# Optimization experiments

Measured on AMD Instinct MI355X. Metric: run time of the kernel, lower is better.

The kernel has to match this reference:

```python
import jax, jax.numpy as jnp
import numpy as np

B, N, D, H = 4096, 257, 16, 128  # batch, agents(incl ego), input_dim, hidden_dim


def setup_inputs() -> dict:
    key = jax.random.key(0)
    k1, k2, k3, k4, k5, k6 = jax.random.split(key, 6)
    x = jax.random.normal(k1, (B, N, D), dtype=jnp.float32)
    # columns 6,7,8 are one-hot type flags (vehicle / pedestrian / barrier)
    tidx = jax.random.randint(k2, (B, N), 0, 3)
    onehot = jax.nn.one_hot(tidx, 3, dtype=jnp.float32)
    x = x.at[:, :, 6:9].set(onehot)
    # Linear params (torch convention: y = x @ W.T + b)
    W_fc = jax.random.normal(k3, (H, D), dtype=jnp.float32) / np.sqrt(D)
    b_fc = jax.random.normal(k4, (H,), dtype=jnp.float32) * 0.01
    W_agg = jax.random.normal(k5, (H, H), dtype=jnp.float32) / np.sqrt(H)
    b_agg = jax.random.normal(k6, (H,), dtype=jnp.float32) * 0.01
    return {"agent_tensor": x, "W_fc": W_fc, "b_fc": b_fc,
            "W_agg": W_agg, "b_agg": b_agg}


def reference(agent_tensor, W_fc, b_fc, W_agg, b_agg):
    x = agent_tensor.astype(jnp.float32)
    ego_pos = x[:, 0, :2]            # [B, 2]
    agents = x[:, 1:, :]             # [B, N-1, D]
    # distance-based weights
    dists = jnp.linalg.norm(agents[:, :, :2] - ego_pos[:, None, :], axis=-1)  # [B, N-1]
    w = 1.0 / (dists + 1.0)
    # vehicle flag multiplies weight by 5 (pedestrian/barrier multipliers are 1.0 -> no-op)
    w = jnp.where(agents[:, :, 6] == 1, w * 5.0, w)
    w = w / (jnp.sum(w, axis=-1, keepdims=True) + 1e-10)
    # per-agent embedding + weighted aggregation
    emb = jax.nn.relu(jnp.einsum('bnd,hd->bnh', agents, W_fc) + b_fc)  # [B, N-1, H]
    agg = jnp.einsum('bn,bnh->bh', w, emb)                              # [B, H]
    return jnp.einsum('bh,gh->bg', jax.nn.relu(agg), W_agg) + b_agg    # [B, H]
```

## Files before the change

### kernel.cpp

```cpp
#include <hip/hip_runtime.h>


typedef _Float16 half_t;
typedef half_t f16x4 __attribute__((ext_vector_type(4)));
typedef float f32x4 __attribute__((ext_vector_type(4)));

__global__ __launch_bounds__(256, 4) void agg_kernel(
    const float* __restrict__ x,
    const float* __restrict__ Wfc,
    const float* __restrict__ bfc,
    half_t* __restrict__ agg_out)
{
    const int t    = threadIdx.x;
    const int lane = t & 63;
    const int wv   = t >> 6;
    const int b    = blockIdx.x * 4 + wv;
    const int lr   = lane & 15;
    const int lc   = lane >> 4;

    __shared__ float wls[4][256];

    const float* xb = x + (size_t)b * (257 * 16);

    float dxv[4], dyv[4], f6[4];
    #pragma unroll
    for (int i = 0; i < 4; ++i) {
        const float* ar = xb + (size_t)(1 + lane + 64 * i) * 16;
        const float2 p = *(const float2*)ar;
        dxv[i] = p.x; dyv[i] = p.y; f6[i] = ar[6];
    }
    const float2 ego = *(const float2*)xb;

    f16x4 afr[16];
    #pragma unroll
    for (int tm = 0; tm < 16; ++tm) {
        const float4 av = *(const float4*)(xb + (size_t)(1 + tm * 16 + lr) * 16 + lc * 4);
        afr[tm] = (f16x4){(half_t)av.x, (half_t)av.y, (half_t)av.z, (half_t)av.w};
    }

    f16x4 bf[8];
    float cbias[8];
    #pragma unroll
    for (int ct = 0; ct < 8; ++ct) {
        const int col = ct * 16 + lr;
        const float4 v = *(const float4*)(Wfc + col * 16 + lc * 4);
        bf[ct] = (f16x4){(half_t)v.x, (half_t)v.y, (half_t)v.z, (half_t)v.w};
        cbias[ct] = bfc[col];
    }

    float wq[4];
    float wsum = 0.f;
    #pragma unroll
    for (int i = 0; i < 4; ++i) {
        const float dx = dxv[i] - ego.x, dy = dyv[i] - ego.y;
        float w = 1.0f / (sqrtf(dx * dx + dy * dy) + 1.0f);
        if (f6[i] == 1.0f) w *= 5.0f;
        wq[i] = w; wsum += w;
    }
    #pragma unroll
    for (int off = 32; off > 0; off >>= 1) wsum += __shfl_xor(wsum, off);
    const float inv = 1.0f / (wsum + 1e-10f);
    #pragma unroll
    for (int i = 0; i < 4; ++i) wls[wv][lane + 64 * i] = wq[i] * inv;

    float pacc[8] = {0.f, 0.f, 0.f, 0.f, 0.f, 0.f, 0.f, 0.f};
    #pragma unroll
    for (int tm = 0; tm < 16; ++tm) {
        const float4 w4 = *(const float4*)(&wls[wv][tm * 16 + lc * 4]);
        #pragma unroll
        for (int ct = 0; ct < 8; ++ct) {
            const f32x4 c = (f32x4){cbias[ct], cbias[ct], cbias[ct], cbias[ct]};
            const f32x4 d = __builtin_amdgcn_mfma_f32_16x16x16f16(afr[tm], bf[ct], c, 0, 0, 0);
            pacc[ct] = fmaf(w4.x, fmaxf(d[0], 0.f), pacc[ct]);
            pacc[ct] = fmaf(w4.y, fmaxf(d[1], 0.f), pacc[ct]);
            pacc[ct] = fmaf(w4.z, fmaxf(d[2], 0.f), pacc[ct]);
            pacc[ct] = fmaf(w4.w, fmaxf(d[3], 0.f), pacc[ct]);
        }
    }

    #pragma unroll
    for (int ct = 0; ct < 8; ++ct) {
        float p = pacc[ct];
        p += __shfl_xor(p, 16);
        p += __shfl_xor(p, 32);
        pacc[ct] = p;
    }
    if (lane < 16) {
        #pragma unroll
        for (int ct = 0; ct < 8; ++ct)
            agg_out[(size_t)b * 128 + ct * 16 + lane] = (half_t)fmaxf(pacc[ct], 0.f);
    }
}

__global__ __launch_bounds__(256) void out_kernel(
    const half_t* __restrict__ agg,
    const float* __restrict__ Wagg,
    const float* __restrict__ bagg,
    float* __restrict__ out)
{
    const int blk  = blockIdx.x;
    const int t    = threadIdx.x;
    const int lane = t & 63;
    const int wv   = t >> 6;
    const int lr   = lane & 15;
    const int lc   = lane >> 4;
    const int row0 = blk * 16;

    f32x4 acc[2];
    #pragma unroll
    for (int ci = 0; ci < 2; ++ci) {
        const int col = (wv * 2 + ci) * 16 + lr;
        const float bb = bagg[col];
        acc[ci] = (f32x4){bb, bb, bb, bb};
    }
    #pragma unroll
    for (int kk = 0; kk < 8; ++kk) {
        const int k0 = kk * 16 + lc * 4;
        const f16x4 a = *(const f16x4*)(agg + (size_t)(row0 + lr) * 128 + k0);
        #pragma unroll
        for (int ci = 0; ci < 2; ++ci) {
            const int col = (wv * 2 + ci) * 16 + lr;
            const float4 v = *(const float4*)(Wagg + col * 128 + k0);
            const f16x4 bfr = (f16x4){(half_t)v.x, (half_t)v.y, (half_t)v.z, (half_t)v.w};
            acc[ci] = __builtin_amdgcn_mfma_f32_16x16x16f16(a, bfr, acc[ci], 0, 0, 0);
        }
    }
    #pragma unroll
    for (int ci = 0; ci < 2; ++ci) {
        const int col = (wv * 2 + ci) * 16 + lr;
        #pragma unroll
        for (int j = 0; j < 4; ++j)
            out[(size_t)(row0 + lc * 4 + j) * 128 + col] = acc[ci][j];
    }
}

extern "C" void kernel_launch(void* const* d_in, const int* in_sizes, int n_in,
                              void* d_out, int out_size, void* d_ws, size_t ws_size,
                              hipStream_t stream) {
    const float* x    = (const float*)d_in[0];
    const float* Wfc  = (const float*)d_in[1];
    const float* bfc  = (const float*)d_in[2];
    const float* Wagg = (const float*)d_in[3];
    const float* bagg = (const float*)d_in[4];
    float* out = (float*)d_out;
    half_t* agg_ws = (half_t*)d_ws;

    agg_kernel<<<dim3(1024), dim3(256), 0, stream>>>(x, Wfc, bfc, agg_ws);
    out_kernel<<<dim3(256), dim3(256), 0, stream>>>(agg_ws, Wagg, bagg, out);
}
```

Baseline: 36.88 us.

## Defer weight normalization and stream agent tiles through a rotating prefetch buffer

The kernel now writes unnormalized distance weights to shared memory and applies the normalization after the MFMA loop, so the wave reduction no longer sits before the main compute. Agent tiles are loaded into a four-deep rotating register buffer and prefetched four tiles ahead, replacing the up-front load of all sixteen tiles. Bias vectors are also prebuilt outside the loop. The aim is to cut register pressure and overlap global loads with MFMA work, at the cost of a slightly different floating-point summation order.

After: 36.06 us. 1.02x faster.

```diff
diff --git a/kernel.cpp b/kernel.cpp
--- a/kernel.cpp
+++ b/kernel.cpp
@@ -22,55 +22,53 @@
 
     const float* xb = x + (size_t)b * (257 * 16);
 
-    float dxv[4], dyv[4], f6[4];
-    #pragma unroll
-    for (int i = 0; i < 4; ++i) {
-        const float* ar = xb + (size_t)(1 + lane + 64 * i) * 16;
-        const float2 p = *(const float2*)ar;
-        dxv[i] = p.x; dyv[i] = p.y; f6[i] = ar[6];
-    }
-    const float2 ego = *(const float2*)xb;
-
-    f16x4 afr[16];
-    #pragma unroll
-    for (int tm = 0; tm < 16; ++tm) {
-        const float4 av = *(const float4*)(xb + (size_t)(1 + tm * 16 + lr) * 16 + lc * 4);
-        afr[tm] = (f16x4){(half_t)av.x, (half_t)av.y, (half_t)av.z, (half_t)av.w};
+    float wq[4];
+    {
+        float2 p[4]; float f6[4];
+        #pragma unroll
+        for (int i = 0; i < 4; ++i) {
+            const float* ar = xb + (size_t)(1 + lane + 64 * i) * 16;
+            p[i] = *(const float2*)ar;
+            f6[i] = ar[6];
+        }
+        const float2 ego = *(const float2*)xb;
+        #pragma unroll
+        for (int i = 0; i < 4; ++i) {
+            const float dx = p[i].x - ego.x, dy = p[i].y - ego.y;
+            float w = 1.0f / (sqrtf(dx * dx + dy * dy) + 1.0f);
+            if (f6[i] == 1.0f) w *= 5.0f;
+            wq[i] = w;
+            wls[wv][lane + 64 * i] = w;
+        }
     }
 
     f16x4 bf[8];
-    float cbias[8];
+    f32x4 cvec[8];
     #pragma unroll
     for (int ct = 0; ct < 8; ++ct) {
         const int col = ct * 16 + lr;
         const float4 v = *(const float4*)(Wfc + col * 16 + lc * 4);
         bf[ct] = (f16x4){(half_t)v.x, (half_t)v.y, (half_t)v.z, (half_t)v.w};
-        cbias[ct] = bfc[col];
+        const float bb = bfc[col];
+        cvec[ct] = (f32x4){bb, bb, bb, bb};
     }
 
-    float wq[4];
-    float wsum = 0.f;
+    float pacc[8] = {0.f, 0.f, 0.f, 0.f, 0.f, 0.f, 0.f, 0.f};
+    float4 abuf[4];
     #pragma unroll
-    for (int i = 0; i < 4; ++i) {
-        const float dx = dxv[i] - ego.x, dy = dyv[i] - ego.y;
-        float w = 1.0f / (sqrtf(dx * dx + dy * dy) + 1.0f);
-        if (f6[i] == 1.0f) w *= 5.0f;
-        wq[i] = w; wsum += w;
-    }
-    #pragma unroll
-    for (int off = 32; off > 0; off >>= 1) wsum += __shfl_xor(wsum, off);
-    const float inv = 1.0f / (wsum + 1e-10f);
-    #pragma unroll
-    for (int i = 0; i < 4; ++i) wls[wv][lane + 64 * i] = wq[i] * inv;
+    for (int i = 0; i < 4; ++i)
+        abuf[i] = *(const float4*)(xb + (size_t)(1 + i * 16 + lr) * 16 + lc * 4);
 
-    float pacc[8] = {0.f, 0.f, 0.f, 0.f, 0.f, 0.f, 0.f, 0.f};
     #pragma unroll
     for (int tm = 0; tm < 16; ++tm) {
+        const float4 av = abuf[tm & 3];
+        if (tm < 12)
+            abuf[tm & 3] = *(const float4*)(xb + (size_t)(1 + (tm + 4) * 16 + lr) * 16 + lc * 4);
+        const f16x4 a = (f16x4){(half_t)av.x, (half_t)av.y, (half_t)av.z, (half_t)av.w};
         const float4 w4 = *(const float4*)(&wls[wv][tm * 16 + lc * 4]);
         #pragma unroll
         for (int ct = 0; ct < 8; ++ct) {
-            const f32x4 c = (f32x4){cbias[ct], cbias[ct], cbias[ct], cbias[ct]};
-            const f32x4 d = __builtin_amdgcn_mfma_f32_16x16x16f16(afr[tm], bf[ct], c, 0, 0, 0);
+            const f32x4 d = __builtin_amdgcn_mfma_f32_16x16x16f16(a, bf[ct], cvec[ct], 0, 0, 0);
             pacc[ct] = fmaf(w4.x, fmaxf(d[0], 0.f), pacc[ct]);
             pacc[ct] = fmaf(w4.y, fmaxf(d[1], 0.f), pacc[ct]);
             pacc[ct] = fmaf(w4.z, fmaxf(d[2], 0.f), pacc[ct]);
@@ -78,12 +76,17 @@
         }
     }
 
+    float wsum = wq[0] + wq[1] + wq[2] + wq[3];
+    #pragma unroll
+    for (int off = 32; off > 0; off >>= 1) wsum += __shfl_xor(wsum, off);
+    const float inv = 1.0f / (wsum + 1e-10f);
+
     #pragma unroll
     for (int ct = 0; ct < 8; ++ct) {
         float p = pacc[ct];
         p += __shfl_xor(p, 16);
         p += __shfl_xor(p, 32);
-        pacc[ct] = p;
+        pacc[ct] = p * inv;
     }
     if (lane < 16) {
         #pragma unroll
```

## Split agents across two waves, use 32x32 MFMA, defer normalization and bias

Applied to the files above, without the earlier changes.

Each batch row is now handled by two waves, each covering half of the 256 agents. The embedding uses the 32x32x16 f16 MFMA with a zero accumulator and clamps at -bias instead of adding the bias first. Each wave writes unnormalized partial sums and its weight sum to fp32 workspace. The second kernel combines the two halves, applies the normalization and the weighted bias (sum of weights is 1), then runs a 16x16x32 MFMA. The aim is more parallelism and less per-wave register and VALU work, at the cost of twice as much fp32 workspace traffic between the kernels.

Measured after the change: 30.47 us. 17.4% less time.

```diff
diff --git a/kernel.cpp b/kernel.cpp
--- a/kernel.cpp
+++ b/kernel.cpp
@@ -2,136 +2,159 @@
 
 
 typedef _Float16 half_t;
-typedef half_t f16x4 __attribute__((ext_vector_type(4)));
+typedef half_t f16x8 __attribute__((ext_vector_type(8)));
 typedef float f32x4 __attribute__((ext_vector_type(4)));
+typedef float f32x16 __attribute__((ext_vector_type(16)));
 
-__global__ __launch_bounds__(256, 4) void agg_kernel(
+__global__ __launch_bounds__(256, 5) void agg_kernel(
     const float* __restrict__ x,
     const float* __restrict__ Wfc,
     const float* __restrict__ bfc,
-    half_t* __restrict__ agg_out)
+    float* __restrict__ p_ws,
+    float* __restrict__ s_ws)
 {
     const int t    = threadIdx.x;
     const int lane = t & 63;
     const int wv   = t >> 6;
-    const int b    = blockIdx.x * 4 + wv;
-    const int lr   = lane & 15;
-    const int lc   = lane >> 4;
+    const int W    = blockIdx.x * 4 + wv;
+    const int b    = W >> 1;
+    const int hf   = W & 1;
+    const int lm   = lane & 31;
+    const int hi   = lane >> 5;
 
-    __shared__ float wls[4][256];
+    __shared__ float wls[4][128];
 
     const float* xb = x + (size_t)b * (257 * 16);
+    const int row0 = 1 + hf * 128;
 
-    float dxv[4], dyv[4], f6[4];
+    float4 a0[4], a1[4];
     #pragma unroll
-    for (int i = 0; i < 4; ++i) {
-        const float* ar = xb + (size_t)(1 + lane + 64 * i) * 16;
-        const float2 p = *(const float2*)ar;
-        dxv[i] = p.x; dyv[i] = p.y; f6[i] = ar[6];
+    for (int tm = 0; tm < 4; ++tm) {
+        const float* rp = xb + (size_t)(row0 + tm * 32 + lm) * 16 + hi * 8;
+        a0[tm] = *(const float4*)rp;
+        a1[tm] = *(const float4*)(rp + 4);
     }
+
+    f16x8 bfr[4];
+    #pragma unroll
+    for (int ct = 0; ct < 4; ++ct) {
+        const float* wp = Wfc + (size_t)(ct * 32 + lm) * 16 + hi * 8;
+        const float4 w0 = *(const float4*)wp;
+        const float4 w1 = *(const float4*)(wp + 4);
+        bfr[ct] = (f16x8){(half_t)w0.x, (half_t)w0.y, (half_t)w0.z, (half_t)w0.w,
+                          (half_t)w1.x, (half_t)w1.y, (half_t)w1.z, (half_t)w1.w};
+    }
+
+    float nb[4];
+    #pragma unroll
+    for (int ct = 0; ct < 4; ++ct) nb[ct] = -bfc[ct * 32 + lm];
+
     const float2 ego = *(const float2*)xb;
 
-    f16x4 afr[16];
-    #pragma unroll
-    for (int tm = 0; tm < 16; ++tm) {
-        const float4 av = *(const float4*)(xb + (size_t)(1 + tm * 16 + lr) * 16 + lc * 4);
-        afr[tm] = (f16x4){(half_t)av.x, (half_t)av.y, (half_t)av.z, (half_t)av.w};
-    }
-
-    f16x4 bf[8];
-    float cbias[8];
-    #pragma unroll
-    for (int ct = 0; ct < 8; ++ct) {
-        const int col = ct * 16 + lr;
-        const float4 v = *(const float4*)(Wfc + col * 16 + lc * 4);
-        bf[ct] = (f16x4){(half_t)v.x, (half_t)v.y, (half_t)v.z, (half_t)v.w};
-        cbias[ct] = bfc[col];
-    }
-
-    float wq[4];
     float wsum = 0.f;
-    #pragma unroll
-    for (int i = 0; i < 4; ++i) {
-        const float dx = dxv[i] - ego.x, dy = dyv[i] - ego.y;
-        float w = 1.0f / (sqrtf(dx * dx + dy * dy) + 1.0f);
-        if (f6[i] == 1.0f) w *= 5.0f;
-        wq[i] = w; wsum += w;
+    if (hi == 0) {
+        #pragma unroll
+        for (int tm = 0; tm < 4; ++tm) {
+            const float dx = a0[tm].x - ego.x;
+            const float dy = a0[tm].y - ego.y;
+            float w = 1.0f / (sqrtf(dx * dx + dy * dy) + 1.0f);
+            if (a1[tm].z == 1.0f) w *= 5.0f;
+            wls[wv][tm * 32 + lm] = w;
+            wsum += w;
+        }
     }
     #pragma unroll
     for (int off = 32; off > 0; off >>= 1) wsum += __shfl_xor(wsum, off);
-    const float inv = 1.0f / (wsum + 1e-10f);
+
+    f16x8 afr[4];
     #pragma unroll
-    for (int i = 0; i < 4; ++i) wls[wv][lane + 64 * i] = wq[i] * inv;
+    for (int tm = 0; tm < 4; ++tm)
+        afr[tm] = (f16x8){(half_t)a0[tm].x, (half_t)a0[tm].y, (half_t)a0[tm].z, (half_t)a0[tm].w,
+                          (half_t)a1[tm].x, (half_t)a1[tm].y, (half_t)a1[tm].z, (half_t)a1[tm].w};
 
-    float pacc[8] = {0.f, 0.f, 0.f, 0.f, 0.f, 0.f, 0.f, 0.f};
+    float pacc[4] = {0.f, 0.f, 0.f, 0.f};
     #pragma unroll
-    for (int tm = 0; tm < 16; ++tm) {
-        const float4 w4 = *(const float4*)(&wls[wv][tm * 16 + lc * 4]);
+    for (int tm = 0; tm < 4; ++tm) {
+        float4 w4[4];
         #pragma unroll
-        for (int ct = 0; ct < 8; ++ct) {
-            const f32x4 c = (f32x4){cbias[ct], cbias[ct], cbias[ct], cbias[ct]};
-            const f32x4 d = __builtin_amdgcn_mfma_f32_16x16x16f16(afr[tm], bf[ct], c, 0, 0, 0);
-            pacc[ct] = fmaf(w4.x, fmaxf(d[0], 0.f), pacc[ct]);
-            pacc[ct] = fmaf(w4.y, fmaxf(d[1], 0.f), pacc[ct]);
-            pacc[ct] = fmaf(w4.z, fmaxf(d[2], 0.f), pacc[ct]);
-            pacc[ct] = fmaf(w4.w, fmaxf(d[3], 0.f), pacc[ct]);
+        for (int q = 0; q < 4; ++q)
+            w4[q] = *(const float4*)(&wls[wv][tm * 32 + q * 8 + hi * 4]);
+        #pragma unroll
+        for (int ct = 0; ct < 4; ++ct) {
+            f32x16 zc = {};
+            const f32x16 d = __builtin_amdgcn_mfma_f32_32x32x16_f16(afr[tm], bfr[ct], zc, 0, 0, 0);
+            #pragma unroll
+            for (int r = 0; r < 16; ++r)
+                pacc[ct] = fmaf(w4[r >> 2][r & 3], fmaxf(d[r], nb[ct]), pacc[ct]);
         }
     }
 
     #pragma unroll
-    for (int ct = 0; ct < 8; ++ct) {
-        float p = pacc[ct];
-        p += __shfl_xor(p, 16);
-        p += __shfl_xor(p, 32);
-        pacc[ct] = p;
-    }
-    if (lane < 16) {
+    for (int ct = 0; ct < 4; ++ct) pacc[ct] += __shfl_xor(pacc[ct], 32);
+    if (hi == 0) {
+        float* pp = p_ws + ((size_t)b * 2 + hf) * 128;
         #pragma unroll
-        for (int ct = 0; ct < 8; ++ct)
-            agg_out[(size_t)b * 128 + ct * 16 + lane] = (half_t)fmaxf(pacc[ct], 0.f);
+        for (int ct = 0; ct < 4; ++ct) pp[ct * 32 + lm] = pacc[ct];
+        if (lane == 0) s_ws[b * 2 + hf] = wsum;
     }
 }
 
-__global__ __launch_bounds__(256) void out_kernel(
-    const half_t* __restrict__ agg,
+__global__ __launch_bounds__(256, 4) void out_kernel(
+    const float* __restrict__ p_ws,
+    const float* __restrict__ s_ws,
+    const float* __restrict__ bfc,
     const float* __restrict__ Wagg,
     const float* __restrict__ bagg,
     float* __restrict__ out)
 {
-    const int blk  = blockIdx.x;
     const int t    = threadIdx.x;
     const int lane = t & 63;
     const int wv   = t >> 6;
+    const int j    = blockIdx.x * 4 + wv;
+    const int mt   = j >> 3;
+    const int ct   = j & 7;
     const int lr   = lane & 15;
-    const int lc   = lane >> 4;
-    const int row0 = blk * 16;
+    const int lq   = lane >> 4;
 
-    f32x4 acc[2];
+    const int brow = mt * 16 + lr;
+    const float2 s2 = *(const float2*)(s_ws + brow * 2);
+    const float inv = 1.0f / (s2.x + s2.y + 1e-10f);
+
+    const int col = ct * 16 + lr;
+    const float bb = bagg[col];
+    f32x4 acc = (f32x4){bb, bb, bb, bb};
+
+    const float* pbase = p_ws + (size_t)brow * 256;
+    const float* wrow  = Wagg + (size_t)col * 128;
+
     #pragma unroll
-    for (int ci = 0; ci < 2; ++ci) {
-        const int col = (wv * 2 + ci) * 16 + lr;
-        const float bb = bagg[col];
-        acc[ci] = (f32x4){bb, bb, bb, bb};
+    for (int kk = 0; kk < 4; ++kk) {
+        const int k0 = kk * 32 + lq * 8;
+        const float4 p00 = *(const float4*)(pbase + k0);
+        const float4 p01 = *(const float4*)(pbase + k0 + 4);
+        const float4 p10 = *(const float4*)(pbase + 128 + k0);
+        const float4 p11 = *(const float4*)(pbase + 128 + k0 + 4);
+        const float4 bf0 = *(const float4*)(bfc + k0);
+        const float4 bf1 = *(const float4*)(bfc + k0 + 4);
+        const f16x8 afr = (f16x8){
+            (half_t)fmaxf(fmaf(p00.x + p10.x, inv, bf0.x), 0.f),
+            (half_t)fmaxf(fmaf(p00.y + p10.y, inv, bf0.y), 0.f),
+            (half_t)fmaxf(fmaf(p00.z + p10.z, inv, bf0.z), 0.f),
+            (half_t)fmaxf(fmaf(p00.w + p10.w, inv, bf0.w), 0.f),
+            (half_t)fmaxf(fmaf(p01.x + p11.x, inv, bf1.x), 0.f),
+            (half_t)fmaxf(fmaf(p01.y + p11.y, inv, bf1.y), 0.f),
+            (half_t)fmaxf(fmaf(p01.z + p11.z, inv, bf1.z), 0.f),
+            (half_t)fmaxf(fmaf(p01.w + p11.w, inv, bf1.w), 0.f)};
+        const float4 wg0 = *(const float4*)(wrow + k0);
+        const float4 wg1 = *(const float4*)(wrow + k0 + 4);
+        const f16x8 bfr = (f16x8){(half_t)wg0.x, (half_t)wg0.y, (half_t)wg0.z, (half_t)wg0.w,
+                                  (half_t)wg1.x, (half_t)wg1.y, (half_t)wg1.z, (half_t)wg1.w};
+        acc = __builtin_amdgcn_mfma_f32_16x16x32_f16(afr, bfr, acc, 0, 0, 0);
     }
+
     #pragma unroll
-    for (int kk = 0; kk < 8; ++kk) {
-        const int k0 = kk * 16 + lc * 4;
-        const f16x4 a = *(const f16x4*)(agg + (size_t)(row0 + lr) * 128 + k0);
-        #pragma unroll
-        for (int ci = 0; ci < 2; ++ci) {
-            const int col = (wv * 2 + ci) * 16 + lr;
-            const float4 v = *(const float4*)(Wagg + col * 128 + k0);
-            const f16x4 bfr = (f16x4){(half_t)v.x, (half_t)v.y, (half_t)v.z, (half_t)v.w};
-            acc[ci] = __builtin_amdgcn_mfma_f32_16x16x16f16(a, bfr, acc[ci], 0, 0, 0);
-        }
-    }
-    #pragma unroll
-    for (int ci = 0; ci < 2; ++ci) {
-        const int col = (wv * 2 + ci) * 16 + lr;
-        #pragma unroll
-        for (int j = 0; j < 4; ++j)
-            out[(size_t)(row0 + lc * 4 + j) * 128 + col] = acc[ci][j];
-    }
+    for (int jj = 0; jj < 4; ++jj)
+        out[(size_t)(mt * 16 + lq * 4 + jj) * 128 + col] = acc[jj];
 }
 
 extern "C" void kernel_launch(void* const* d_in, const int* in_sizes, int n_in,
@@ -143,8 +166,10 @@
     const float* Wagg = (const float*)d_in[3];
     const float* bagg = (const float*)d_in[4];
     float* out = (float*)d_out;
-    half_t* agg_ws = (half_t*)d_ws;
 
-    agg_kernel<<<dim3(1024), dim3(256), 0, stream>>>(x, Wfc, bfc, agg_ws);
-    out_kernel<<<dim3(256), dim3(256), 0, stream>>>(agg_ws, Wagg, bagg, out);
+    float* p_ws = (float*)d_ws;
+    float* s_ws = p_ws + (size_t)4096 * 256;
+
+    agg_kernel<<<dim3(2048), dim3(256), 0, stream>>>(x, Wfc, bfc, p_ws, s_ws);
+    out_kernel<<<dim3(512), dim3(256), 0, stream>>>(p_ws, s_ws, bfc, Wagg, bagg, out);
 }
```
